# Kernel tuning notes

Hardware: AMD Instinct MI355X
Metric: run time of the kernel (lower is better)

The kernel has to match this reference:

```python
import jax, jax.numpy as jnp
import numpy as np

B, T, D, O = 16, 1024, 1024, 10  # broadcast in original requires T == D

def setup_inputs() -> dict:
    key = jax.random.key(0)
    k1, k2, k3 = jax.random.split(key, 3)
    logits = jax.random.normal(k1, (B, T, D), dtype=jnp.float32)
    decision = jax.random.uniform(k2, (B, T, O), dtype=jnp.float32)  # unused by forward math
    W = jax.random.normal(k3, (O, D), dtype=jnp.float32) * 0.02  # attention.weight
    b = jnp.zeros((O,), dtype=jnp.float32)                       # attention.bias
    return {"logits": logits, "decision": decision, "W": W, "b": b}

def reference(logits, decision, W, b):
    outputdim = W.shape[0]
    # w_x = softmax(Linear(logits)/outputdim, dim=1)  -> softmax over time T
    scores = (jnp.einsum('btd,od->bto', logits, W) + b) / outputdim  # (B,T,O)
    w_x = jax.nn.softmax(scores, axis=1)
    # Original materializes h[b,i,o,t] = logits[b,t,i] * w_x[b,i,o] (needs T==D),
    # then flattens (o,t) and sums over dim 1 (i). Equivalent contraction:
    # out[b,o,t] = sum_i logits[b,t,i] * w_x[b,i,o]
    out = jnp.einsum('bti,bio->bot', logits, w_x)  # (B,O,T)
    return out.reshape(logits.shape[0], -1)        # (B, O*T)
```

## Files before the change

kernel.cpp:

```cpp
#include <hip/hip_runtime.h>

#define BB 16
#define TT 1024
#define DD 1024
#define OO 10

template <bool FIRST>
__global__ __launch_bounds__(256) void gemm10_kernel(
    const float* __restrict__ X,
    const float* __restrict__ Wt,
    const float* __restrict__ bias,
    float* __restrict__ Y)
{
    __shared__ float4 sW4[OO * 256];
    __shared__ float  part[4][32][OO];
    __shared__ float  zred[OO];

    const int b   = blockIdx.y;
    const int t0  = blockIdx.x * 32;
    const int tid = threadIdx.x;

    {
        const float4* src = (const float4*)(Wt + (FIRST ? 0 : (size_t)b * OO * TT));
#pragma unroll
        for (int c = 0; c < 10; ++c)
            sW4[c * 256 + tid] = src[c * 256 + tid];
    }
    __syncthreads();

    const int w    = tid >> 6;
    const int lane = tid & 63;
    const int l    = lane & 7;
    const int g    = lane >> 3;
    const int dofs = w * 256 + l * 4;

    if (!FIRST) {
#pragma unroll
        for (int k = 0; k < 3; ++k) {
            const int o = w + 4 * k;
            if (o < OO) {
                float s = 0.f;
#pragma unroll
                for (int q = 0; q < 4; ++q) {
                    const float4 v = sW4[o * 256 + lane * 4 + q];
                    s += v.x + v.y + v.z + v.w;
                }
#pragma unroll
                for (int off = 32; off > 0; off >>= 1)
                    s += __shfl_down(s, off, 64);
                if (lane == 0) zred[o] = s;
            }
        }
    }

    const float* xp[4];
#pragma unroll
    for (int j = 0; j < 4; ++j)
        xp[j] = X + ((size_t)b * TT + t0 + g + 8 * j) * DD + dofs;
    const float* sWl = (const float*)sW4 + dofs;

    float acc[4][OO];
#pragma unroll
    for (int j = 0; j < 4; ++j)
#pragma unroll
        for (int o = 0; o < OO; ++o) acc[j][o] = 0.f;

    float4 x0[4], x1[4];
#pragma unroll
    for (int j = 0; j < 4; ++j) {
        x0[j] = *(const float4*)(xp[j]);
        x1[j] = *(const float4*)(xp[j] + 32);
    }

#pragma unroll 1
    for (int it = 0; it < 8; it += 2) {
        float4 c0[4];
#pragma unroll
        for (int j = 0; j < 4; ++j) c0[j] = x0[j];
        if (it < 6) {
#pragma unroll
            for (int j = 0; j < 4; ++j)
                x0[j] = *(const float4*)(xp[j] + (it + 2) * 32);
        }
        {
            const float* wp = sWl + it * 32;
#pragma unroll
            for (int o = 0; o < OO; ++o) {
                const float4 wv = *(const float4*)(wp + o * DD);
#pragma unroll
                for (int j = 0; j < 4; ++j)
                    acc[j][o] += c0[j].x * wv.x + c0[j].y * wv.y +
                                 c0[j].z * wv.z + c0[j].w * wv.w;
            }
        }
#pragma unroll
        for (int j = 0; j < 4; ++j) c0[j] = x1[j];
        if (it < 5) {
#pragma unroll
            for (int j = 0; j < 4; ++j)
                x1[j] = *(const float4*)(xp[j] + (it + 3) * 32);
        }
        {
            const float* wp = sWl + (it + 1) * 32;
#pragma unroll
            for (int o = 0; o < OO; ++o) {
                const float4 wv = *(const float4*)(wp + o * DD);
#pragma unroll
                for (int j = 0; j < 4; ++j)
                    acc[j][o] += c0[j].x * wv.x + c0[j].y * wv.y +
                                 c0[j].z * wv.z + c0[j].w * wv.w;
            }
        }
    }

#pragma unroll
    for (int j = 0; j < 4; ++j) {
#pragma unroll
        for (int o = 0; o < OO; ++o) {
            float v = acc[j][o];
            v += __shfl_down(v, 4, 8);
            v += __shfl_down(v, 2, 8);
            v += __shfl_down(v, 1, 8);
            if (l == 0) part[w][j * 8 + g][o] = v;
        }
    }
    __syncthreads();

    for (int idx = tid; idx < 32 * OO; idx += 256) {
        const int row = idx / OO;
        const int o   = idx % OO;
        float v = part[0][row][o] + part[1][row][o] +
                  part[2][row][o] + part[3][row][o];
        if (FIRST) {
            Y[((size_t)b * OO + o) * TT + (t0 + row)] =
                __expf((v + bias[o]) * (1.0f / OO));
        } else {
            Y[((size_t)b * OO + o) * TT + (t0 + row)] = v / zred[o];
        }
    }
}

extern "C" void kernel_launch(void* const* d_in, const int* in_sizes, int n_in,
                              void* d_out, int out_size, void* d_ws, size_t ws_size,
                              hipStream_t stream)
{
    const float* logits = (const float*)d_in[0];
    const float* W    = (const float*)d_in[2];
    const float* bias = (const float*)d_in[3];
    float* out = (float*)d_out;
    float* u   = (float*)d_ws;

    dim3 grid(TT / 32, BB);
    gemm10_kernel<true><<<grid, 256, 0, stream>>>(logits, W, bias, u);
    gemm10_kernel<false><<<grid, 256, 0, stream>>>(logits, u, nullptr, out);
}
```

Baseline: 121.0 us.

## Fuse both GEMM passes into one cooperative kernel with grid-wide sync

Replaces the two back-to-back kernel launches with a single cooperative kernel that runs both phases. A grid-wide barrier separates computing the exp scores from consuming them. The intermediate is stored in the output buffer instead of the workspace, and the second phase syncs the grid again before overwriting it. This removes one launch and the gap between kernels, at the cost of grid-sync overhead and the requirement that all 512 blocks be co-resident; if the cooperative launch fails it falls back to the two-kernel path.

Result: slower. 226.4 us (+87.1%).

```diff
diff --git a/kernel.cpp b/kernel.cpp
--- a/kernel.cpp
+++ b/kernel.cpp
@@ -1,9 +1,157 @@
 #include <hip/hip_runtime.h>
+#include <hip/hip_cooperative_groups.h>
+
+namespace cg = cooperative_groups;
 
 #define BB 16
 #define TT 1024
 #define DD 1024
 #define OO 10
+
+__global__ __launch_bounds__(256) void fused_kernel(
+    const float* __restrict__ X,
+    const float* __restrict__ W,
+    const float* __restrict__ bias,
+    float* __restrict__ Y)
+{
+    cg::grid_group gg = cg::this_grid();
+
+    __shared__ float4 sW4[OO * 256];
+    __shared__ float  part[4][32][OO];
+    __shared__ float  zred[OO];
+
+    const int b   = blockIdx.y;
+    const int t0  = blockIdx.x * 32;
+    const int tid = threadIdx.x;
+
+    const int w    = tid >> 6;
+    const int lane = tid & 63;
+    const int l    = lane & 7;
+    const int g    = lane >> 3;
+    const int dofs = w * 256 + l * 4;
+
+    const float* xp[4];
+#pragma unroll
+    for (int j = 0; j < 4; ++j)
+        xp[j] = X + ((size_t)b * TT + t0 + g + 8 * j) * DD + dofs;
+    const float* sWl = (const float*)sW4 + dofs;
+    float* const uslab = Y + (size_t)b * OO * TT;
+
+#pragma unroll
+    for (int phase = 0; phase < 2; ++phase) {
+        {
+            const float4* src = (phase == 0) ? (const float4*)W
+                                             : (const float4*)uslab;
+#pragma unroll
+            for (int c = 0; c < 10; ++c)
+                sW4[c * 256 + tid] = src[c * 256 + tid];
+        }
+        __syncthreads();
+
+        if (phase == 1) {
+#pragma unroll
+            for (int k = 0; k < 3; ++k) {
+                const int o = w + 4 * k;
+                if (o < OO) {
+                    float s = 0.f;
+#pragma unroll
+                    for (int q = 0; q < 4; ++q) {
+                        const float4 v = sW4[o * 256 + lane * 4 + q];
+                        s += v.x + v.y + v.z + v.w;
+                    }
+#pragma unroll
+                    for (int off = 32; off > 0; off >>= 1)
+                        s += __shfl_down(s, off, 64);
+                    if (lane == 0) zred[o] = s;
+                }
+            }
+        }
+
+        float acc[4][OO];
+#pragma unroll
+        for (int j = 0; j < 4; ++j)
+#pragma unroll
+            for (int o = 0; o < OO; ++o) acc[j][o] = 0.f;
+
+        float4 x0[4], x1[4];
+#pragma unroll
+        for (int j = 0; j < 4; ++j) {
+            x0[j] = *(const float4*)(xp[j]);
+            x1[j] = *(const float4*)(xp[j] + 32);
+        }
+
+#pragma unroll 1
+        for (int it = 0; it < 8; it += 2) {
+            float4 c0[4];
+#pragma unroll
+            for (int j = 0; j < 4; ++j) c0[j] = x0[j];
+            if (it < 6) {
+#pragma unroll
+                for (int j = 0; j < 4; ++j)
+                    x0[j] = *(const float4*)(xp[j] + (it + 2) * 32);
+            }
+            {
+                const float* wp = sWl + it * 32;
+#pragma unroll
+                for (int o = 0; o < OO; ++o) {
+                    const float4 wv = *(const float4*)(wp + o * DD);
+#pragma unroll
+                    for (int j = 0; j < 4; ++j)
+                        acc[j][o] += c0[j].x * wv.x + c0[j].y * wv.y +
+                                     c0[j].z * wv.z + c0[j].w * wv.w;
+                }
+            }
+#pragma unroll
+            for (int j = 0; j < 4; ++j) c0[j] = x1[j];
+            if (it < 5) {
+#pragma unroll
+                for (int j = 0; j < 4; ++j)
+                    x1[j] = *(const float4*)(xp[j] + (it + 3) * 32);
+            }
+            {
+                const float* wp = sWl + (it + 1) * 32;
+#pragma unroll
+                for (int o = 0; o < OO; ++o) {
+                    const float4 wv = *(const float4*)(wp + o * DD);
+#pragma unroll
+                    for (int j = 0; j < 4; ++j)
+                        acc[j][o] += c0[j].x * wv.x + c0[j].y * wv.y +
+                                     c0[j].z * wv.z + c0[j].w * wv.w;
+                }
+            }
+        }
+
+#pragma unroll
+        for (int j = 0; j < 4; ++j) {
+#pragma unroll
+            for (int o = 0; o < OO; ++o) {
+                float v = acc[j][o];
+                v += __shfl_down(v, 4, 8);
+                v += __shfl_down(v, 2, 8);
+                v += __shfl_down(v, 1, 8);
+                if (l == 0) part[w][j * 8 + g][o] = v;
+            }
+        }
+        __syncthreads();
+
+        if (phase == 1) gg.sync();
+
+        for (int idx = tid; idx < 32 * OO; idx += 256) {
+            const int row = idx / OO;
+            const int o   = idx % OO;
+            float v = part[0][row][o] + part[1][row][o] +
+                      part[2][row][o] + part[3][row][o];
+            if (phase == 0) {
+                Y[((size_t)b * OO + o) * TT + (t0 + row)] =
+                    __expf((v + bias[o]) * (1.0f / OO));
+            } else {
+                Y[((size_t)b * OO + o) * TT + (t0 + row)] = v / zred[o];
+            }
+        }
+
+        if (phase == 0) gg.sync();
+    }
+}
 
 template <bool FIRST>
 __global__ __launch_bounds__(256) void gemm10_kernel(
@@ -148,9 +296,18 @@
     const float* W    = (const float*)d_in[2];
     const float* bias = (const float*)d_in[3];
     float* out = (float*)d_out;
-    float* u   = (float*)d_ws;
 
     dim3 grid(TT / 32, BB);
-    gemm10_kernel<true><<<grid, 256, 0, stream>>>(logits, W, bias, u);
-    gemm10_kernel<false><<<grid, 256, 0, stream>>>(logits, u, nullptr, out);
+    dim3 block(256);
+
+    void* args[] = { (void*)&logits, (void*)&W, (void*)&bias, (void*)&out };
+    hipError_t err = hipLaunchCooperativeKernel(
+        (const void*)fused_kernel, grid, block, args, 0, stream);
+
+    if (err != hipSuccess) {
+        (void)hipGetLastError();
+        float* u = (float*)d_ws;
+        gemm10_kernel<true><<<grid, block, 0, stream>>>(logits, W, bias, u);
+        gemm10_kernel<false><<<grid, block, 0, stream>>>(logits, u, nullptr, out);
+    }
 }
```
